# Kernel optimization log

Measured on AMD Instinct MI355X. Metric: run time of the kernel, lower is better.

The kernel has to match this reference:

```python
import jax, jax.numpy as jnp
import numpy as np


def _khot_counts(ids, vocab_size, pad_id):
    # ids: [N, L] int -> counts: [N, V] float32, pad tokens contribute 0
    N, L = ids.shape
    w = (ids != pad_id).astype(jnp.float32)
    return jnp.zeros((N, vocab_size), jnp.float32).at[jnp.arange(N)[:, None], ids].add(w)


def setup_inputs() -> dict:
    key = jax.random.key(0)
    B, K, L_src, L_cand, V = 64, 16, 64, 32, 50257
    k1, k2 = jax.random.split(key)
    src_ids = jax.random.randint(k1, (B, L_src), 0, V)
    candidates = jax.random.randint(k2, (B, K, L_cand), 0, V)
    return {"candidates": candidates, "src_ids": src_ids, "vocab_size": V, "pad_id": 0}


def reference(candidates, src_ids, vocab_size, pad_id):
    B, K, Lc = candidates.shape
    # k-hot (token count) vectors, pad ignored
    refs = _khot_counts(src_ids, vocab_size, pad_id)                  # [B, V]
    cands = _khot_counts(candidates.reshape(B * K, Lc), vocab_size, pad_id)
    cands = cands.reshape(B, K, vocab_size)                           # [B, K, V]
    # cosine similarity -> dissimilarity score
    dots = jnp.einsum('bv,bkv->bk', refs, cands)                      # [B, K]
    denom = jnp.linalg.norm(refs, axis=-1, keepdims=True) * jnp.linalg.norm(cands, axis=-1)
    scores = 1.0 - dots / denom                                       # [B, K]
    # sort descending, gather candidates in sorted order
    order = jnp.argsort(-scores, axis=-1)                             # [B, K]
    scores_sorted = jnp.take_along_axis(scores, order, axis=-1)
    cand_sorted = jnp.take_along_axis(candidates, order[:, :, None], axis=1)
    output = cand_sorted[:, 0, :]                                     # top1: [B, Lc]
    lengths = jnp.sum(output != pad_id, axis=-1)                      # [B]
    return output, lengths, scores_sorted
```

## Files before the change

### kernel.cpp

```cpp
#include <hip/hip_runtime.h>


#define NB 64
#define NK 16
#define LS 64
#define LC 32

__global__ __launch_bounds__(256) void rerank_kernel(const int* __restrict__ cand,
                                                     const int* __restrict__ src,
                                                     float* __restrict__ out) {
    __shared__ int   s_src[LS];
    __shared__ int   s_cand[NK * LC];
    __shared__ float s_tokdot[NK * LC];
    __shared__ float s_tokssc[NK * LC];
    __shared__ float s_scores[NK];
    __shared__ float s_ssr;
    __shared__ int   s_best;

    const int b = blockIdx.x;
    const int t = threadIdx.x;

    if (t < LS) s_src[t] = src[b * LS + t];
    for (int idx = t; idx < NK * LC; idx += 256) s_cand[idx] = cand[b * NK * LC + idx];
    __syncthreads();

    if (t < LS) {
        int c = s_src[t];
        int cnt = 0;
        if (c != 0) {
            #pragma unroll
            for (int j = 0; j < LS; ++j) cnt += (s_src[j] == c) ? 1 : 0;
        }
        #pragma unroll
        for (int off = 32; off > 0; off >>= 1) cnt += __shfl_down(cnt, off, 64);
        if (t == 0) s_ssr = (float)cnt;
    }

    for (int idx = t; idx < NK * LC; idx += 256) {
        int c = s_cand[idx];
        int k = idx >> 5;
        int dotc = 0, sscc = 0;
        if (c != 0) {
            #pragma unroll
            for (int i = 0; i < LS; ++i) dotc += (s_src[i] == c) ? 1 : 0;
            #pragma unroll
            for (int j = 0; j < LC; ++j) sscc += (s_cand[(k << 5) + j] == c) ? 1 : 0;
        }
        s_tokdot[idx] = (float)dotc;
        s_tokssc[idx] = (float)sscc;
    }
    __syncthreads();

    if (t < NK) {
        float dot = 0.f, ssc = 0.f;
        #pragma unroll
        for (int j = 0; j < LC; ++j) {
            dot += s_tokdot[(t << 5) + j];
            ssc += s_tokssc[(t << 5) + j];
        }
        float denom = sqrtf(s_ssr) * sqrtf(ssc);
        s_scores[t] = 1.0f - dot / denom;
    }
    __syncthreads();

    if (t < NK) {
        float sc = s_scores[t];
        int rank = 0;
        #pragma unroll
        for (int j = 0; j < NK; ++j) {
            float sj = s_scores[j];
            rank += ((sj > sc) || (sj == sc && j < t)) ? 1 : 0;
        }
        if (rank == 0) s_best = t;
        out[NB * LC + NB + b * NK + rank] = sc;
    }
    __syncthreads();

    const int best = s_best;
    if (t < LC) {
        out[b * LC + t] = (float)s_cand[best * LC + t];
    }
    if (t == 0) {
        int len = 0;
        #pragma unroll
        for (int j = 0; j < LC; ++j) len += (s_cand[best * LC + j] != 0) ? 1 : 0;
        out[NB * LC + b] = (float)len;
    }
}

extern "C" void kernel_launch(void* const* d_in, const int* in_sizes, int n_in,
                              void* d_out, int out_size, void* d_ws, size_t ws_size,
                              hipStream_t stream) {
    const int* cand = (const int*)d_in[0];
    const int* src  = (const int*)d_in[1];
    float* out = (float*)d_out;
    rerank_kernel<<<NB, 256, 0, stream>>>(cand, src, out);
}
```

Measured before the change: 62.66 us.

## Use one thread per candidate token, vectorize LDS compares, reduce with shuffles

Raises the block size to 512 so each thread handles exactly one candidate token instead of looping twice. Token match counting now reads shared memory as int4 vectors, and the per-candidate sums are reduced with 32-lane xor shuffles instead of going through a shared-memory array and a serial 32-element loop. This removes the loop, a shared-memory round trip and a serial summation. The cost is a larger block. The kernel is tiny and launch-dominated, so the gain may be marginal.

```diff
diff --git a/kernel.cpp b/kernel.cpp
--- a/kernel.cpp
+++ b/kernel.cpp
@@ -6,13 +6,13 @@
 #define LS 64
 #define LC 32
 
-__global__ __launch_bounds__(256) void rerank_kernel(const int* __restrict__ cand,
+__global__ __launch_bounds__(512) void rerank_kernel(const int* __restrict__ cand,
                                                      const int* __restrict__ src,
                                                      float* __restrict__ out) {
     __shared__ int   s_src[LS];
     __shared__ int   s_cand[NK * LC];
-    __shared__ float s_tokdot[NK * LC];
-    __shared__ float s_tokssc[NK * LC];
+    __shared__ int   s_dot[NK];
+    __shared__ int   s_ssc[NK];
     __shared__ float s_scores[NK];
     __shared__ float s_ssr;
     __shared__ int   s_best;
@@ -21,43 +21,53 @@
     const int t = threadIdx.x;
 
     if (t < LS) s_src[t] = src[b * LS + t];
-    for (int idx = t; idx < NK * LC; idx += 256) s_cand[idx] = cand[b * NK * LC + idx];
+    s_cand[t] = cand[b * NK * LC + t];
     __syncthreads();
 
     if (t < LS) {
-        int c = s_src[t];
+        int cs = s_src[t];
         int cnt = 0;
-        if (c != 0) {
+        if (cs != 0) {
+            const int4* s4 = (const int4*)s_src;
             #pragma unroll
-            for (int j = 0; j < LS; ++j) cnt += (s_src[j] == c) ? 1 : 0;
+            for (int i = 0; i < LS / 4; ++i) {
+                int4 v = s4[i];
+                cnt += (v.x == cs) + (v.y == cs) + (v.z == cs) + (v.w == cs);
+            }
         }
         #pragma unroll
-        for (int off = 32; off > 0; off >>= 1) cnt += __shfl_down(cnt, off, 64);
+        for (int off = 32; off > 0; off >>= 1) cnt += __shfl_xor(cnt, off, 64);
         if (t == 0) s_ssr = (float)cnt;
     }
 
-    for (int idx = t; idx < NK * LC; idx += 256) {
-        int c = s_cand[idx];
-        int k = idx >> 5;
-        int dotc = 0, sscc = 0;
-        if (c != 0) {
-            #pragma unroll
-            for (int i = 0; i < LS; ++i) dotc += (s_src[i] == c) ? 1 : 0;
-            #pragma unroll
-            for (int j = 0; j < LC; ++j) sscc += (s_cand[(k << 5) + j] == c) ? 1 : 0;
+    const int c = s_cand[t];
+    const int k = t >> 5;
+    int dotc = 0, sscc = 0;
+    if (c != 0) {
+        const int4* s4 = (const int4*)s_src;
+        #pragma unroll
+        for (int i = 0; i < LS / 4; ++i) {
+            int4 v = s4[i];
+            dotc += (v.x == c) + (v.y == c) + (v.z == c) + (v.w == c);
         }
-        s_tokdot[idx] = (float)dotc;
-        s_tokssc[idx] = (float)sscc;
+        const int4* r4 = (const int4*)(s_cand + (k << 5));
+        #pragma unroll
+        for (int j = 0; j < LC / 4; ++j) {
+            int4 v = r4[j];
+            sscc += (v.x == c) + (v.y == c) + (v.z == c) + (v.w == c);
+        }
     }
+    #pragma unroll
+    for (int off = 16; off > 0; off >>= 1) {
+        dotc += __shfl_xor(dotc, off, 32);
+        sscc += __shfl_xor(sscc, off, 32);
+    }
+    if ((t & 31) == 0) { s_dot[k] = dotc; s_ssc[k] = sscc; }
     __syncthreads();
 
     if (t < NK) {
-        float dot = 0.f, ssc = 0.f;
-        #pragma unroll
-        for (int j = 0; j < LC; ++j) {
-            dot += s_tokdot[(t << 5) + j];
-            ssc += s_tokssc[(t << 5) + j];
-        }
+        float dot = (float)s_dot[t];
+        float ssc = (float)s_ssc[t];
         float denom = sqrtf(s_ssr) * sqrtf(ssc);
         s_scores[t] = 1.0f - dot / denom;
     }
@@ -77,13 +87,11 @@
     __syncthreads();
 
     const int best = s_best;
-    if (t < LC) {
-        out[b * LC + t] = (float)s_cand[best * LC + t];
-    }
+    if (t < LC) out[b * LC + t] = (float)s_cand[(best << 5) + t];
     if (t == 0) {
         int len = 0;
         #pragma unroll
-        for (int j = 0; j < LC; ++j) len += (s_cand[best * LC + j] != 0) ? 1 : 0;
+        for (int j = 0; j < LC; ++j) len += (s_cand[(best << 5) + j] != 0) ? 1 : 0;
         out[NB * LC + b] = (float)len;
     }
 }
@@ -94,5 +102,5 @@
     const int* cand = (const int*)d_in[0];
     const int* src  = (const int*)d_in[1];
     float* out = (float*)d_out;
-    rerank_kernel<<<NB, 256, 0, stream>>>(cand, src, out);
+    rerank_kernel<<<NB, 512, 0, stream>>>(cand, src, out);
 }
```

After: 60.99 us. -2.7%, faster.
